# Performance work log

Measured on AMD Instinct MI355X. Metric: run time of the kernel, lower is better.

The kernel has to match this reference:

```python
import jax, jax.numpy as jnp
import numpy as np

MARGIN = 1.0
B, D, T = 8192, 256, 100000


def setup_inputs() -> dict:
    key = jax.random.key(0)
    k1, k2 = jax.random.split(key)
    embeddings = jax.random.normal(k1, (B, D), dtype=jnp.float32)
    triplets = jax.random.randint(k2, (T, 3), 0, B, dtype=jnp.int64)
    return {"embeddings": embeddings, "triplets": triplets}


def _rowwise_l2(x, y):
    # Equivalent to torch.diagonal(torch.cdist(x, y)) without the NxN waste.
    d = x - y
    return jnp.sqrt(jnp.sum(d * d, axis=-1))


def reference(embeddings, triplets):
    anchor = embeddings[triplets[:, 0]]      # [T, D]
    positives = embeddings[triplets[:, 1]]   # [T, D]
    negatives = embeddings[triplets[:, 2]]   # [T, D]
    ap = _rowwise_l2(anchor, positives)
    an = _rowwise_l2(anchor, negatives)
    pn = _rowwise_l2(positives, negatives)
    an_pn = jnp.minimum(an, pn)
    losses = jax.nn.relu(ap - an_pn + MARGIN)
    return (losses.mean(), triplets.shape[0])
```

## Files before the change

kernel.cpp:

```cpp
#include <hip/hip_runtime.h>
#include <hip/hip_bf16.h>
#include <math.h>


__device__ __forceinline__ float bf16_rne(float f) {
    union { float f; unsigned int u; } v;
    v.f = f;
    v.u = (v.u + 0x7FFFu + ((v.u >> 16) & 1u)) & 0xFFFF0000u;
    return v.f;
}

__global__ void triplet_partial(const float* __restrict__ emb,
                                const int* __restrict__ tri,
                                int T, int B,
                                float* __restrict__ partials) {
    const int lane = threadIdx.x & 63;
    const int wib  = threadIdx.x >> 6;
    const int wpb  = blockDim.x >> 6;
    const int gw   = blockIdx.x * wpb + wib;
    const int nw   = gridDim.x * wpb;

    float local = 0.0f;

    for (int t = gw; t < T; t += nw) {
        const int a = tri[3 * t + 0];
        const int p = tri[3 * t + 1];
        const int n = tri[3 * t + 2];
        const bool ok = (unsigned)a < (unsigned)B &&
                        (unsigned)p < (unsigned)B &&
                        (unsigned)n < (unsigned)B;
        if (ok) {
            const float4 va = *((const float4*)(emb + (size_t)a * 256) + lane);
            const float4 vp = *((const float4*)(emb + (size_t)p * 256) + lane);
            const float4 vn = *((const float4*)(emb + (size_t)n * 256) + lane);

            float dap = 0.f, dan = 0.f, dpn = 0.f, d;
            d = va.x - vp.x; dap += d * d;
            d = va.y - vp.y; dap += d * d;
            d = va.z - vp.z; dap += d * d;
            d = va.w - vp.w; dap += d * d;
            d = va.x - vn.x; dan += d * d;
            d = va.y - vn.y; dan += d * d;
            d = va.z - vn.z; dan += d * d;
            d = va.w - vn.w; dan += d * d;
            d = vp.x - vn.x; dpn += d * d;
            d = vp.y - vn.y; dpn += d * d;
            d = vp.z - vn.z; dpn += d * d;
            d = vp.w - vn.w; dpn += d * d;

            #pragma unroll
            for (int off = 32; off > 0; off >>= 1) {
                dap += __shfl_xor(dap, off);
                dan += __shfl_xor(dan, off);
                dpn += __shfl_xor(dpn, off);
            }

            if (lane == 0) {
                const float l = sqrtf(dap) - fminf(sqrtf(dan), sqrtf(dpn)) + 1.0f;
                if (l > 0.0f && l < 1000.0f) local += l;
            }
        }
    }

    __shared__ float s[8];
    if (lane == 0) s[wib] = local;
    __syncthreads();
    if (threadIdx.x == 0) {
        float sum = 0.0f;
        for (int i = 0; i < wpb; ++i) sum += s[i];
        partials[blockIdx.x] = sum;
    }
}

__global__ void triplet_finalize(const float* __restrict__ partials,
                                 int nparts, int T,
                                 float* __restrict__ out) {
    __shared__ float s[256];
    float sum = 0.0f;
    for (int i = threadIdx.x; i < nparts; i += blockDim.x) sum += partials[i];
    s[threadIdx.x] = sum;
    __syncthreads();
    for (int stride = 128; stride > 0; stride >>= 1) {
        if (threadIdx.x < stride) s[threadIdx.x] += s[threadIdx.x + stride];
        __syncthreads();
    }
    if (threadIdx.x == 0) {
        out[0] = s[0] / (float)T;
        out[1] = bf16_rne((float)T);
    }
}

extern "C" void kernel_launch(void* const* d_in, const int* in_sizes, int n_in,
                              void* d_out, int out_size, void* d_ws, size_t ws_size,
                              hipStream_t stream) {
    const float* emb = (const float*)d_in[0];
    const int*   tri = (const int*)d_in[1];
    const int T = in_sizes[1] / 3;
    const int B = in_sizes[0] / 256;

    float* out = (float*)d_out;
    float* partials = (float*)d_ws;

    const int BLOCKS = 1024, THREADS = 256;
    triplet_partial<<<BLOCKS, THREADS, 0, stream>>>(emb, tri, T, B, partials);
    triplet_finalize<<<1, 256, 0, stream>>>(partials, BLOCKS, T, out);
}
```

Measured before the change: 39.77 us.

## Process four triplets per wavefront with 16-lane subgroups

Splits each 64-lane wavefront into four 16-lane groups, each handling its own triplet. Every lane now loads four float4 values per embedding row instead of one. This raises memory-level parallelism per lane and cuts loop iterations and shuffle-reduction depth per triplet. A wave-level reduction of the per-lane loss accumulators is added at the end. The cost is higher register use and less coalesced access within each individual load instruction.

```diff
diff --git a/kernel.cpp b/kernel.cpp
--- a/kernel.cpp
+++ b/kernel.cpp
@@ -15,52 +15,74 @@
                                 int T, int B,
                                 float* __restrict__ partials) {
     const int lane = threadIdx.x & 63;
+    const int sub  = lane & 15;
+    const int grp  = lane >> 4;
     const int wib  = threadIdx.x >> 6;
     const int wpb  = blockDim.x >> 6;
     const int gw   = blockIdx.x * wpb + wib;
     const int nw   = gridDim.x * wpb;
 
+    const int nquads = (T + 3) >> 2;
     float local = 0.0f;
 
-    for (int t = gw; t < T; t += nw) {
-        const int a = tri[3 * t + 0];
-        const int p = tri[3 * t + 1];
-        const int n = tri[3 * t + 2];
-        const bool ok = (unsigned)a < (unsigned)B &&
-                        (unsigned)p < (unsigned)B &&
-                        (unsigned)n < (unsigned)B;
-        if (ok) {
-            const float4 va = *((const float4*)(emb + (size_t)a * 256) + lane);
-            const float4 vp = *((const float4*)(emb + (size_t)p * 256) + lane);
-            const float4 vn = *((const float4*)(emb + (size_t)n * 256) + lane);
+    for (int q = gw; q < nquads; q += nw) {
+        const int t = 4 * q + grp;
+        float dap = 0.f, dan = 0.f, dpn = 0.f;
+        bool valid = false;
 
-            float dap = 0.f, dan = 0.f, dpn = 0.f, d;
-            d = va.x - vp.x; dap += d * d;
-            d = va.y - vp.y; dap += d * d;
-            d = va.z - vp.z; dap += d * d;
-            d = va.w - vp.w; dap += d * d;
-            d = va.x - vn.x; dan += d * d;
-            d = va.y - vn.y; dan += d * d;
-            d = va.z - vn.z; dan += d * d;
-            d = va.w - vn.w; dan += d * d;
-            d = vp.x - vn.x; dpn += d * d;
-            d = vp.y - vn.y; dpn += d * d;
-            d = vp.z - vn.z; dpn += d * d;
-            d = vp.w - vn.w; dpn += d * d;
+        if (t < T) {
+            const int a = tri[3 * t + 0];
+            const int p = tri[3 * t + 1];
+            const int n = tri[3 * t + 2];
+            valid = (unsigned)a < (unsigned)B &&
+                    (unsigned)p < (unsigned)B &&
+                    (unsigned)n < (unsigned)B;
+            if (valid) {
+                const float4* ra = (const float4*)(emb + (size_t)a * 256) + sub * 4;
+                const float4* rp = (const float4*)(emb + (size_t)p * 256) + sub * 4;
+                const float4* rn = (const float4*)(emb + (size_t)n * 256) + sub * 4;
 
-            #pragma unroll
-            for (int off = 32; off > 0; off >>= 1) {
-                dap += __shfl_xor(dap, off);
-                dan += __shfl_xor(dan, off);
-                dpn += __shfl_xor(dpn, off);
-            }
+                float4 va0 = ra[0], va1 = ra[1], va2 = ra[2], va3 = ra[3];
+                float4 vp0 = rp[0], vp1 = rp[1], vp2 = rp[2], vp3 = rp[3];
+                float4 vn0 = rn[0], vn1 = rn[1], vn2 = rn[2], vn3 = rn[3];
 
-            if (lane == 0) {
-                const float l = sqrtf(dap) - fminf(sqrtf(dan), sqrtf(dpn)) + 1.0f;
-                if (l > 0.0f && l < 1000.0f) local += l;
+                float d;
+                #define ACC(VA, VP, VN) \
+                    d = VA.x - VP.x; dap += d * d; \
+                    d = VA.y - VP.y; dap += d * d; \
+                    d = VA.z - VP.z; dap += d * d; \
+                    d = VA.w - VP.w; dap += d * d; \
+                    d = VA.x - VN.x; dan += d * d; \
+                    d = VA.y - VN.y; dan += d * d; \
+                    d = VA.z - VN.z; dan += d * d; \
+                    d = VA.w - VN.w; dan += d * d; \
+                    d = VP.x - VN.x; dpn += d * d; \
+                    d = VP.y - VN.y; dpn += d * d; \
+                    d = VP.z - VN.z; dpn += d * d; \
+                    d = VP.w - VN.w; dpn += d * d;
+                ACC(va0, vp0, vn0)
+                ACC(va1, vp1, vn1)
+                ACC(va2, vp2, vn2)
+                ACC(va3, vp3, vn3)
+                #undef ACC
             }
         }
+
+        #pragma unroll
+        for (int off = 8; off > 0; off >>= 1) {
+            dap += __shfl_xor(dap, off);
+            dan += __shfl_xor(dan, off);
+            dpn += __shfl_xor(dpn, off);
+        }
+
+        if (sub == 0 && valid) {
+            const float l = sqrtf(dap) - fminf(sqrtf(dan), sqrtf(dpn)) + 1.0f;
+            if (l > 0.0f && l < 1000.0f) local += l;
+        }
     }
+
+    #pragma unroll
+    for (int off = 32; off > 0; off >>= 1) local += __shfl_xor(local, off);
 
     __shared__ float s[8];
     if (lane == 0) s[wib] = local;
```

After: 36.54 us, median of 3. 1.09x faster.
